# Kernel optimization log

Hardware: AMD Instinct MI355X
Metric: run time of the kernel (lower is better)

## Reference

```python
import jax, jax.numpy as jnp
import numpy as np
from math import factorial, pi

IRREPS_L = [0]*32 + [1]*16 + [2]*8 + [3]*8 + [4]*4
LS = sorted(set(IRREPS_L))
DIM = sum(2*l+1 for l in IRREPS_L)

# ---- setup-time numpy: real-SH Wigner matrix of the fixed rotation Rx(-pi/2) ----
# Using the identity Ry(beta) = Rx(-pi/2) Rz(beta) Rx(-pi/2)^T, so
# D_y(beta) = A_l @ Z_l(beta) @ A_l^{-1} with A_l = D_l(Rx(-pi/2)) (fixed constant).

def _assoc_legendre_all(l, x):
    # P_l^m(x) for m = 0..l (Condon-Shortley phase), x ndarray
    res = []
    for m in range(l+1):
        pmm = np.ones_like(x)
        if m > 0:
            somx2 = np.sqrt(np.maximum(1.0 - x*x, 0.0))
            fact = 1.0
            for _ in range(m):
                pmm = -pmm * fact * somx2
                fact += 2.0
        if l == m:
            res.append(pmm); continue
        pmmp1 = x * (2*m+1) * pmm
        if l == m+1:
            res.append(pmmp1); continue
        for ll in range(m+2, l+1):
            pll = ((2*ll-1)*x*pmmp1 - (ll+m-1)*pmm) / (ll-m)
            pmm, pmmp1 = pmmp1, pll
        res.append(pmmp1)
    return res

def _real_sh(l, pts):
    # orthonormal real spherical harmonics, columns ordered m=-l..l
    x, y, z = pts[:, 0], pts[:, 1], pts[:, 2]
    phi = np.arctan2(y, x)
    P = _assoc_legendre_all(l, z)
    cols = []
    for m in range(-l, l+1):
        am = abs(m)
        N = np.sqrt((2*l+1)/(4*pi) * factorial(l-am)/factorial(l+am))
        if m == 0:
            cols.append(N * P[0])
        elif m > 0:
            cols.append(np.sqrt(2.0)*N*P[am]*np.cos(m*phi))
        else:
            cols.append(np.sqrt(2.0)*N*P[am]*np.sin(am*phi))
    return np.stack(cols, axis=1)

def _wigner_of_rotation(l, R):
    # solve D from Y(R x) = D Y(x) via least squares on random unit vectors
    rng = np.random.default_rng(1234 + l)
    v = rng.normal(size=(8*(2*l+1)+16, 3))
    v /= np.linalg.norm(v, axis=1, keepdims=True)
    Yx = _real_sh(l, v)
    Yrx = _real_sh(l, v @ R.T)
    Dt, *_ = np.linalg.lstsq(Yx, Yrx, rcond=None)
    return Dt.T

_RX = np.array([[1., 0., 0.], [0., 0., 1.], [0., -1., 0.]])  # Rx(-pi/2): z -> y
_A = {l: jnp.asarray(_wigner_of_rotation(l, _RX).astype(np.float32)) for l in LS}
_AINV = {l: jnp.asarray(np.linalg.inv(np.asarray(_A[l])).astype(np.float32)) for l in LS}


def _z_rot(l, theta):
    # real-basis z-rotation block: diag cos(m*theta), antidiag -sin(m*theta), m=-l..l
    n = 2*l + 1
    m = jnp.arange(-l, l+1, dtype=theta.dtype)
    ang = m[None, :] * theta[:, None]            # (B, n)
    inds = jnp.arange(n)
    M = jnp.zeros((theta.shape[0], n, n), theta.dtype)
    M = M.at[:, inds, n-1-inds].set(-jnp.sin(ang))
    M = M.at[:, inds, inds].set(jnp.cos(ang))    # center (m=0) overwritten to 1
    return M


def setup_inputs() -> dict:
    key = jax.random.key(0)
    ka, kb, kg = jax.random.split(key, 3)
    B = 2048
    return {
        "alpha": jax.random.normal(ka, (B,), dtype=jnp.float32),
        "beta": jax.random.normal(kb, (B,), dtype=jnp.float32),
        "gamma": jax.random.normal(kg, (B,), dtype=jnp.float32),
    }


def reference(alpha, beta, gamma):
    # D(a,b,c) = Dz(a) Dy(b) Dz(c), Dy(b) = A Zl(b) A^{-1}, block-diag over irreps
    B = alpha.shape[0]
    blocks = {}
    for l in LS:
        Dl = _z_rot(l, alpha) @ _A[l] @ _z_rot(l, beta) @ _AINV[l] @ _z_rot(l, gamma)
        blocks[l] = Dl
    D = jnp.zeros((B, DIM, DIM), alpha.dtype)
    off = 0
    for l in IRREPS_L:
        n = 2*l + 1
        D = D.at[:, off:off+n, off:off+n].set(blocks[l])
        off += n
    return D
```

## Files before the change

### kernel.cpp

```cpp
#include <hip/hip_runtime.h>
#include <cstdint>
#include <cmath>


#define WDIM 212
#define NBLK 165
#define NWRITE 1092
#define SLICE (WDIM * WDIM)
#define SLICE4 (SLICE / 4)

__device__ __constant__ int c_moff[5] = {0, 1, 10, 35, 84};

struct TabM { unsigned char l[NBLK], i[NBLK], j[NBLK]; };
constexpr TabM make_tabM() {
  TabM t{};
  int idx = 0;
  for (int l = 0; l < 5; l++) {
    int n = 2 * l + 1;
    for (int i = 0; i < n; i++)
      for (int j = 0; j < n; j++) {
        t.l[idx] = (unsigned char)l;
        t.i[idx] = (unsigned char)i;
        t.j[idx] = (unsigned char)j;
        idx++;
      }
  }
  return t;
}
__device__ __constant__ TabM c_tabM = make_tabM();

struct TabW { unsigned short off[NWRITE]; unsigned char l[NWRITE], i[NWRITE], j[NWRITE]; };
constexpr TabW make_tabW() {
  TabW t{};
  const int cnt[5] = {32, 16, 8, 8, 4};
  const int start[5] = {0, 32, 80, 120, 176};
  int idx = 0;
  for (int l = 0; l < 5; l++) {
    int n = 2 * l + 1;
    for (int c = 0; c < cnt[l]; c++) {
      int off = start[l] + c * n;
      for (int i = 0; i < n; i++)
        for (int j = 0; j < n; j++) {
          t.off[idx] = (unsigned short)off;
          t.l[idx] = (unsigned char)l;
          t.i[idx] = (unsigned char)i;
          t.j[idx] = (unsigned char)j;
          idx++;
        }
    }
  }
  return t;
}
__device__ __constant__ TabW c_tabW = make_tabW();

__device__ float g_ws[330];

__device__ inline double rnd_double(uint64_t x) {
  x += 0x9E3779B97F4A7C15ull;
  x = (x ^ (x >> 30)) * 0xBF58476D1CE4E5B9ull;
  x = (x ^ (x >> 27)) * 0x94D049BB133111EBull;
  x ^= x >> 31;
  return (double)(x >> 11) * (1.0 / 4503599627370496.0) - 1.0;
}

__device__ void eval_real_sh(int l, const double p[3], double* outv) {
  const double x = p[0], y = p[1], z = p[2];
  const double phi = atan2(y, x);
  double P[5];
  for (int m = 0; m <= l; m++) {
    double pmm = 1.0;
    if (m > 0) {
      double somx2 = sqrt(fmax(1.0 - z * z, 0.0));
      double fct = 1.0;
      for (int k = 0; k < m; k++) { pmm = -pmm * fct * somx2; fct += 2.0; }
    }
    if (l == m) { P[m] = pmm; continue; }
    double pmmp1 = z * (2 * m + 1) * pmm;
    if (l == m + 1) { P[m] = pmmp1; continue; }
    for (int ll = m + 2; ll <= l; ll++) {
      double pll = ((2 * ll - 1) * z * pmmp1 - (ll + m - 1) * pmm) / (double)(ll - m);
      pmm = pmmp1;
      pmmp1 = pll;
    }
    P[m] = pmmp1;
  }
  const double fact[9] = {1, 1, 2, 6, 24, 120, 720, 5040, 40320};
  const double four_pi = 4.0 * 3.14159265358979323846;
  for (int m = -l; m <= l; m++) {
    int am = m < 0 ? -m : m;
    double N = sqrt((2 * l + 1) / four_pi * fact[l - am] / fact[l + am]);
    double v;
    if (m == 0) v = N * P[0];
    else if (m > 0) v = sqrt(2.0) * N * P[am] * cos(m * phi);
    else v = sqrt(2.0) * N * P[am] * sin(am * phi);
    outv[m + l] = v;
  }
}

__global__ __launch_bounds__(320) void wigner_setup() {
  const int l = threadIdx.x >> 6;
  const int lane = threadIdx.x & 63;
  const int n = 2 * l + 1;

  __shared__ double Y[5][48][9];
  __shared__ double Yr[5][48][9];
  __shared__ double G[5][9][18];
  __shared__ double F[5][9];

  if (lane < 48) {
    uint64_t base = ((uint64_t)l * 1024u + (uint64_t)lane) * 4u + 1u;
    double p[3];
    double nrm2 = 0.0;
    for (int c = 0; c < 3; c++) { p[c] = rnd_double(base + (uint64_t)c); nrm2 += p[c] * p[c]; }
    if (nrm2 < 1e-12) { p[0] = 1.0; p[1] = 0.5; p[2] = 0.25; nrm2 = 1.3125; }
    double invn = 1.0 / sqrt(nrm2);
    p[0] *= invn; p[1] *= invn; p[2] *= invn;
    double q[3] = { p[0], p[2], -p[1] };
    eval_real_sh(l, p, &Y[l][lane][0]);
    eval_real_sh(l, q, &Yr[l][lane][0]);
  }
  __syncthreads();

  for (int e = lane; e < 162; e += 64) {
    int r = e / 18, c = e % 18;
    double v;
    if (c < 9) {
      if (r < n && c < n) {
        v = 0.0;
        for (int s = 0; s < 48; s++) v += Y[l][s][r] * Y[l][s][c];
      } else v = (r == c) ? 1.0 : 0.0;
    } else {
      int cc = c - 9;
      if (r < n && cc < n) {
        v = 0.0;
        for (int s = 0; s < 48; s++) v += Y[l][s][r] * Yr[l][s][cc];
      } else v = 0.0;
    }
    G[l][r][c] = v;
  }
  __syncthreads();

  for (int k = 0; k < 9; k++) {
    double ipiv = 1.0 / G[l][k][k];
    if (lane < 18) G[l][k][lane] *= ipiv;
    __syncthreads();
    if (lane < 9) F[l][lane] = G[l][lane][k];
    __syncthreads();
    for (int e = lane; e < 162; e += 64) {
      int r = e / 18, c = e % 18;
      if (r != k) G[l][r][c] -= F[l][r] * G[l][k][c];
    }
    __syncthreads();
  }

  for (int e = lane; e < n * n; e += 64) {
    int i = e / n, j = e % n;
    g_ws[c_moff[l] + e]       = (float)G[l][j][9 + i];
    g_ws[165 + c_moff[l] + e] = (float)G[l][i][9 + j];
  }
}

__global__ __launch_bounds__(256) void wigner_main(const float* __restrict__ alpha,
                                                   const float* __restrict__ beta,
                                                   const float* __restrict__ gamma,
                                                   float* __restrict__ out) {
  const int b = blockIdx.x;
  const int tid = threadIdx.x;
  const float a = alpha[b];
  const float be = beta[b];
  const float g = gamma[b];

  __shared__ float sA[330];
  __shared__ float sT[NBLK];
  __shared__ float sM[NBLK];

  float4* __restrict__ oz = (float4*)(out + (size_t)b * SLICE);
  const float4 z4 = make_float4(0.f, 0.f, 0.f, 0.f);
  #pragma unroll 4
  for (int e = tid; e < SLICE4; e += 256) oz[e] = z4;

  for (int e = tid; e < 330; e += 256) sA[e] = g_ws[e];
  __syncthreads();

  for (int e = tid; e < NBLK; e += 256) {
    int l = c_tabM.l[e], i = c_tabM.i[e], j = c_tabM.j[e];
    int n = 2 * l + 1, moff = c_moff[l];
    int i2 = n - 1 - i;
    float mi = (float)(i - l);
    float sb, cb;
    __sincosf(mi * be, &sb, &cb);
    sT[e] = cb * sA[165 + moff + i * n + j] - sb * sA[165 + moff + i2 * n + j];
  }
  __syncthreads();

  for (int e = tid; e < NBLK; e += 256) {
    int l = c_tabM.l[e], i = c_tabM.i[e], j = c_tabM.j[e];
    int n = 2 * l + 1, moff = c_moff[l];
    float acc = 0.f;
    for (int k = 0; k < n; k++) acc += sA[moff + i * n + k] * sT[moff + k * n + j];
    sM[e] = acc;
  }
  __syncthreads();

  const size_t obase = (size_t)b * SLICE;
  for (int t = tid; t < NWRITE; t += 256) {
    int l = c_tabW.l[t], i = c_tabW.i[t], j = c_tabW.j[t];
    int off = c_tabW.off[t];
    int n = 2 * l + 1, moff = c_moff[l];
    int i2 = n - 1 - i, j2 = n - 1 - j;
    float mi = (float)(i - l), mj = (float)(j - l);
    float sa, ca, sg, cg;
    __sincosf(mi * a, &sa, &ca);
    __sincosf(mj * g, &sg, &cg);
    float r0 = sM[moff + i * n + j] * cg + sM[moff + i * n + j2] * sg;
    float r1 = sM[moff + i2 * n + j] * cg + sM[moff + i2 * n + j2] * sg;
    out[obase + (size_t)(off + i) * WDIM + (off + j)] = ca * r0 - sa * r1;
  }
}

extern "C" void kernel_launch(void* const* d_in, const int* in_sizes, int n_in,
                              void* d_out, int out_size, void* d_ws, size_t ws_size,
                              hipStream_t stream) {
  const float* alpha = (const float*)d_in[0];
  const float* beta  = (const float*)d_in[1];
  const float* gamma = (const float*)d_in[2];
  float* out = (float*)d_out;
  const int B = in_sizes[0];

  wigner_setup<<<1, 320, 0, stream>>>();
  wigner_main<<<B, 256, 0, stream>>>(alpha, beta, gamma, out);
}
```

Measured before the change: 434.4 us.

## Stage block values in shared memory and write full output rows with single vector stores

```diff
diff --git a/kernel.cpp b/kernel.cpp
--- a/kernel.cpp
+++ b/kernel.cpp
@@ -8,6 +8,8 @@
 #define NWRITE 1092
 #define SLICE (WDIM * WDIM)
 #define SLICE4 (SLICE / 4)
+
+typedef float vfloat4 __attribute__((ext_vector_type(4)));
 
 __device__ __constant__ int c_moff[5] = {0, 1, 10, 35, 84};
 
@@ -29,29 +31,45 @@
 }
 __device__ __constant__ TabM c_tabM = make_tabM();
 
-struct TabW { unsigned short off[NWRITE]; unsigned char l[NWRITE], i[NWRITE], j[NWRITE]; };
+struct TabW { unsigned char l[NWRITE], i[NWRITE], j[NWRITE]; };
 constexpr TabW make_tabW() {
   TabW t{};
   const int cnt[5] = {32, 16, 8, 8, 4};
-  const int start[5] = {0, 32, 80, 120, 176};
   int idx = 0;
   for (int l = 0; l < 5; l++) {
     int n = 2 * l + 1;
-    for (int c = 0; c < cnt[l]; c++) {
-      int off = start[l] + c * n;
+    for (int c = 0; c < cnt[l]; c++)
       for (int i = 0; i < n; i++)
         for (int j = 0; j < n; j++) {
-          t.off[idx] = (unsigned short)off;
           t.l[idx] = (unsigned char)l;
           t.i[idx] = (unsigned char)i;
           t.j[idx] = (unsigned char)j;
           idx++;
         }
-    }
   }
   return t;
 }
 __device__ __constant__ TabW c_tabW = make_tabW();
+
+struct RowTab { unsigned int v[WDIM]; };
+constexpr RowTab make_rows() {
+  RowTab t{};
+  const int cnt[5] = {32, 16, 8, 8, 4};
+  int row = 0, d = 0;
+  for (int li = 0; li < 5; li++) {
+    int n = 2 * li + 1;
+    for (int c = 0; c < cnt[li]; c++) {
+      int off = row;
+      for (int i = 0; i < n; i++) {
+        t.v[row] = (unsigned)(d | (off << 12) | (n << 20));
+        d += n;
+        row++;
+      }
+    }
+  }
+  return t;
+}
+__device__ __constant__ RowTab c_rows = make_rows();
 
 __device__ float g_ws[330];
 
@@ -65,7 +83,20 @@
 
 __device__ void eval_real_sh(int l, const double p[3], double* outv) {
   const double x = p[0], y = p[1], z = p[2];
-  const double phi = atan2(y, x);
+  double rho2 = x * x + y * y;
+  double cm[5], sm[5];
+  cm[0] = 1.0; sm[0] = 0.0;
+  {
+    double c1, s1;
+    if (rho2 > 1e-300) {
+      double ir = 1.0 / sqrt(rho2);
+      c1 = x * ir; s1 = y * ir;
+    } else { c1 = 1.0; s1 = 0.0; }
+    for (int m = 1; m <= l; m++) {
+      cm[m] = cm[m - 1] * c1 - sm[m - 1] * s1;
+      sm[m] = sm[m - 1] * c1 + cm[m - 1] * s1;
+    }
+  }
   double P[5];
   for (int m = 0; m <= l; m++) {
     double pmm = 1.0;
@@ -91,8 +122,8 @@
     double N = sqrt((2 * l + 1) / four_pi * fact[l - am] / fact[l + am]);
     double v;
     if (m == 0) v = N * P[0];
-    else if (m > 0) v = sqrt(2.0) * N * P[am] * cos(m * phi);
-    else v = sqrt(2.0) * N * P[am] * sin(am * phi);
+    else if (m > 0) v = sqrt(2.0) * N * P[am] * cm[am];
+    else v = sqrt(2.0) * N * P[am] * sm[am];
     outv[m + l] = v;
   }
 }
@@ -173,13 +204,11 @@
   __shared__ float sA[330];
   __shared__ float sT[NBLK];
   __shared__ float sM[NBLK];
-
-  float4* __restrict__ oz = (float4*)(out + (size_t)b * SLICE);
-  const float4 z4 = make_float4(0.f, 0.f, 0.f, 0.f);
-  #pragma unroll 4
-  for (int e = tid; e < SLICE4; e += 256) oz[e] = z4;
+  __shared__ float sD[NWRITE];
+  __shared__ unsigned int sRow[WDIM];
 
   for (int e = tid; e < 330; e += 256) sA[e] = g_ws[e];
+  if (tid < WDIM) sRow[tid] = c_rows.v[tid];
   __syncthreads();
 
   for (int e = tid; e < NBLK; e += 256) {
@@ -202,10 +231,8 @@
   }
   __syncthreads();
 
-  const size_t obase = (size_t)b * SLICE;
   for (int t = tid; t < NWRITE; t += 256) {
     int l = c_tabW.l[t], i = c_tabW.i[t], j = c_tabW.j[t];
-    int off = c_tabW.off[t];
     int n = 2 * l + 1, moff = c_moff[l];
     int i2 = n - 1 - i, j2 = n - 1 - j;
     float mi = (float)(i - l), mj = (float)(j - l);
@@ -214,7 +241,27 @@
     __sincosf(mj * g, &sg, &cg);
     float r0 = sM[moff + i * n + j] * cg + sM[moff + i * n + j2] * sg;
     float r1 = sM[moff + i2 * n + j] * cg + sM[moff + i2 * n + j2] * sg;
-    out[obase + (size_t)(off + i) * WDIM + (off + j)] = ca * r0 - sa * r1;
+    sD[t] = ca * r0 - sa * r1;
+  }
+  __syncthreads();
+
+  vfloat4* __restrict__ oz = (vfloat4*)(out + (size_t)b * SLICE);
+  #pragma unroll 2
+  for (int e = tid; e < SLICE4; e += 256) {
+    int r = e / 53;
+    int c0 = (e - r * 53) * 4;
+    unsigned info = sRow[r];
+    int dstart = info & 0xFFF;
+    int off = (info >> 12) & 0xFF;
+    int n = (info >> 20) & 0xF;
+    vfloat4 v = (vfloat4)(0.f);
+    int i0 = c0 - off;
+    #pragma unroll
+    for (int q = 0; q < 4; q++) {
+      int idx = i0 + q;
+      if ((unsigned)idx < (unsigned)n) v[q] = sD[dstart + idx];
+    }
+    __builtin_nontemporal_store(v, oz + e);
   }
 }
 
```

New measurement: 397.0 us. 8.6% less time.
